# Kernel optimization log

Measured on AMD Instinct MI355X. Metric: run time of the kernel, lower is better.

Reference implementation:

```python
import jax, jax.numpy as jnp
import numpy as np
import math

N_QUBITS = 8
N_LAYERS = 2
EMBED = 512
HEADS = 64
B, T = 2, 1024


def _ry(state, theta, wire, off):
    # state: (batch?, 2, 2, ..., 2); theta: scalar or (N,)
    ax = off + wire
    st = jnp.moveaxis(state, ax, -1)
    s0, s1 = st[..., 0], st[..., 1]
    half = jnp.asarray(theta) * 0.5
    c, s = jnp.cos(half), jnp.sin(half)
    if c.ndim:  # batched angles -> broadcast over remaining qubit axes
        c = c.reshape((-1,) + (1,) * (s0.ndim - 1))
        s = s.reshape((-1,) + (1,) * (s0.ndim - 1))
    new = jnp.stack([c * s0 - s * s1, s * s0 + c * s1], axis=-1)
    return jnp.moveaxis(new, -1, ax)


def _cnot(state, cw, tw, off):
    st = jnp.moveaxis(state, (off + cw, off + tw), (-2, -1))
    new = jnp.stack([st[..., 0, :], st[..., 1, ::-1]], axis=-2)
    return jnp.moveaxis(new, (-2, -1), (off + cw, off + tw))


def _entangling_state(params):
    # Fixed-parameter block applied to |0...0>: single shared statevector.
    n = N_QUBITS
    psi = jnp.zeros((2,) * n, dtype=params.dtype).at[(0,) * n].set(1.0)
    for l in range(N_LAYERS):
        for q in range(n):
            psi = _ry(psi, params[l, q], q, 0)
        for q in range(n - 1):
            psi = _cnot(psi, q, q + 1, 0)
        psi = _cnot(psi, n - 1, 0, 0)
    return psi


def _quantum_heads(angles, params):
    # angles: (N, n_qubits) data-encoding RY angles; returns (N, n_qubits) <Z_q>.
    n = N_QUBITS
    psi0 = _entangling_state(params)
    state = jnp.broadcast_to(psi0, (angles.shape[0],) + (2,) * n)
    for q in range(n):
        state = _ry(state, angles[:, q], q, 1)
    probs = state * state  # real statevector -> probabilities
    zs = []
    for q in range(n):
        axes = tuple(a for a in range(1, n + 1) if a != q + 1)
        m = probs.sum(axes)  # (N, 2)
        zs.append(m[:, 0] - m[:, 1])
    return jnp.stack(zs, axis=-1)


def setup_inputs() -> dict:
    key = jax.random.key(0)
    kx, kq, kk, kv, kp = jax.random.split(key, 5)
    scale = 1.0 / math.sqrt(EMBED)
    return {
        "x": jax.random.normal(kx, (B, T, EMBED), dtype=jnp.float32),
        "Wq": jax.random.normal(kq, (EMBED, EMBED), dtype=jnp.float32) * scale,
        "Wk": jax.random.normal(kk, (EMBED, EMBED), dtype=jnp.float32) * scale,
        "Wv": jax.random.normal(kv, (EMBED, EMBED), dtype=jnp.float32) * scale,
        "params": jax.random.normal(kp, (N_LAYERS, N_QUBITS), dtype=jnp.float32),
    }


def reference(x, Wq, Wk, Wv, params):
    Bx, Tx, E = x.shape
    head_dim = E // HEADS
    q = x @ Wq.T
    k = x @ Wk.T
    v = x @ Wv.T
    # NOTE: attention on the full embed dim (no head split), scaled by sqrt(E).
    scores = jnp.einsum("bte,bse->bts", q, k) / jnp.sqrt(jnp.asarray(E, x.dtype))
    weights = jax.nn.softmax(scores, axis=-1)
    out = jnp.einsum("bts,bse->bte", weights, v)
    heads = out.reshape(Bx, Tx, HEADS, head_dim)[..., :N_QUBITS]
    angles = heads.reshape(-1, N_QUBITS)  # (B*T*HEADS, n_qubits)
    z = _quantum_heads(angles, params)
    return z.reshape(Bx, Tx, HEADS * N_QUBITS)
```

## Files before the change

### kernel.cpp

```cpp
#include <hip/hip_runtime.h>
#include <math.h>

typedef __attribute__((ext_vector_type(8))) short bf16x8;
typedef __attribute__((ext_vector_type(4))) float f32x4;

__device__ __forceinline__ ushort f2b(float f) {
    unsigned u = __float_as_uint(f);
    return (ushort)((u + 0x7FFFu + ((u >> 16) & 1u)) >> 16);
}

__device__ __forceinline__ void gl16(const ushort* g, ushort* l) {
    __builtin_amdgcn_global_load_lds((const __attribute__((address_space(1))) void*)g,
                                     (__attribute__((address_space(3))) void*)l, 16, 0, 0);
}

__device__ __forceinline__ void wait_pipe() { asm volatile("s_waitcnt vmcnt(4) lgkmcnt(0)" ::: "memory"); }
__device__ __forceinline__ void wait_all()  { asm volatile("s_waitcnt vmcnt(0) lgkmcnt(0)" ::: "memory"); }

__device__ __forceinline__ void stage64(const ushort* g, int ld, ushort* lds,
                                        int w, int lane) {
    const int rsub = lane >> 3;
    const size_t coff = (size_t)(((lane & 7) ^ (rsub & 7)) * 8);
#pragma unroll
    for (int ii = 0; ii < 2; ++ii) {
        const int i = w * 2 + ii;
        gl16(g + (size_t)(i * 8 + rsub) * ld + coff, lds + i * 512);
    }
}

__device__ __forceinline__ bf16x8 frag(const ushort* lds, int row0, int c, int lane) {
    const int r = row0 + (lane & 15);
    const int slot = (c * 4 + (lane >> 4)) ^ (r & 7);
    return *(const bf16x8*)(lds + (size_t)r * 64 + slot * 8);
}

__device__ __forceinline__ void compute64(const ushort* As, const ushort* Bs,
                                          f32x4 acc[2][2], int lane, int wr, int wc) {
#pragma unroll
    for (int c = 0; c < 2; ++c) {
        bf16x8 a[2], b[2];
#pragma unroll
        for (int f = 0; f < 2; ++f) {
            a[f] = frag(As, wr * 32 + f * 16, c, lane);
            b[f] = frag(Bs, wc * 32 + f * 16, c, lane);
        }
#pragma unroll
        for (int i = 0; i < 2; ++i)
#pragma unroll
            for (int j = 0; j < 2; ++j)
                acc[i][j] = __builtin_amdgcn_mfma_f32_16x16x32_bf16(a[i], b[j], acc[i][j], 0, 0, 0);
    }
}

__global__ __launch_bounds__(256) void cvtq_kernel(const float* __restrict__ x,
                                                   const float* __restrict__ wq,
                                                   const float* __restrict__ wk,
                                                   const float* __restrict__ wv,
                                                   const float* __restrict__ params,
                                                   ushort* __restrict__ xb,
                                                   ushort* __restrict__ wqb,
                                                   ushort* __restrict__ wkb,
                                                   ushort* __restrict__ wvb,
                                                   float* __restrict__ ab) {
    const int tid = threadIdx.x;
    if (blockIdx.y < 4) {
        const int z = blockIdx.y;
        const float* src = (z == 0) ? x : (z == 1) ? wq : (z == 2) ? wk : wv;
        ushort* dst = (z == 0) ? xb : (z == 1) ? wqb : (z == 2) ? wkb : wvb;
        const int n = (z == 0) ? (2048 * 512) : (512 * 512);
        const int i = (blockIdx.x * 256 + tid) * 8;
        if (i >= n) return;
        float4 v0 = *(const float4*)(src + i);
        float4 v1 = *(const float4*)(src + i + 4);
        ushort t[8] = {f2b(v0.x), f2b(v0.y), f2b(v0.z), f2b(v0.w),
                       f2b(v1.x), f2b(v1.y), f2b(v1.z), f2b(v1.w)};
        *(uint4*)(dst + i) = *(uint4*)t;
        return;
    }
    if (blockIdx.x != 0) return;
    __shared__ float st[256];
    __shared__ float red[64];
    st[tid] = (tid == 0) ? 1.0f : 0.0f;
    __syncthreads();
    for (int l = 0; l < 2; ++l) {
        for (int q = 0; q < 8; ++q) {
            float h = 0.5f * params[l * 8 + q];
            float c = cosf(h), s = sinf(h);
            int str = 1 << (7 - q);
            if ((tid & str) == 0) {
                float s0 = st[tid], s1 = st[tid + str];
                st[tid]       = c * s0 - s * s1;
                st[tid + str] = s * s0 + c * s1;
            }
            __syncthreads();
        }
        for (int q = 0; q < 8; ++q) {
            int cw = q, tw = (q + 1) & 7;
            int cs = 1 << (7 - cw), ts = 1 << (7 - tw);
            if ((tid & cs) && !(tid & ts)) {
                float a = st[tid], b = st[tid ^ ts];
                st[tid] = b;
                st[tid ^ ts] = a;
            }
            __syncthreads();
        }
    }
    const float amp = st[tid];
    float v[16];
#pragma unroll
    for (int q = 0; q < 8; ++q) {
        int str = 1 << (7 - q);
        v[q]     = amp * amp * ((tid & str) ? -1.0f : 1.0f);
        v[8 + q] = ((tid & str) == 0) ? 2.0f * amp * st[tid ^ str] : 0.0f;
    }
#pragma unroll
    for (int off = 32; off; off >>= 1)
#pragma unroll
        for (int q = 0; q < 16; ++q) v[q] += __shfl_xor(v[q], off);
    const int lane = tid & 63, wid = tid >> 6;
    if (lane == 0)
#pragma unroll
        for (int q = 0; q < 16; ++q) red[wid * 16 + q] = v[q];
    __syncthreads();
    if (tid < 16) ab[tid] = red[tid] + red[16 + tid] + red[32 + tid] + red[48 + tid];
}

__global__ __launch_bounds__(256) void qkv_mfma(const ushort* __restrict__ xb,
                                                const ushort* __restrict__ wqb,
                                                const ushort* __restrict__ wkb,
                                                const ushort* __restrict__ wvb,
                                                ushort* __restrict__ qb,
                                                ushort* __restrict__ kb,
                                                ushort* __restrict__ vT) {
    __shared__ ushort lds[3][2 * 64 * 64];
    const int tid = threadIdx.x, lane = tid & 63, w = tid >> 6;
    const int wr = w >> 1, wc = w & 1;
    const int z = blockIdx.z;
    int m0, n0, ldc;
    const ushort *A, *B;
    ushort* C;
    if (z < 2) {
        m0 = blockIdx.x << 6;  n0 = blockIdx.y << 6;
        A = xb;  B = (z == 0) ? wqb : wkb;  C = (z == 0) ? qb : kb;  ldc = 512;
    } else {
        m0 = blockIdx.y << 6;  n0 = blockIdx.x << 6;
        A = wvb;  B = xb;  C = vT;  ldc = 2048;
    }
    const ushort* Ap = A + (size_t)m0 * 512;
    const ushort* Bp = B + (size_t)n0 * 512;
    stage64(Ap, 512, lds[0], w, lane);
    stage64(Bp, 512, lds[0] + 4096, w, lane);
    stage64(Ap + 64, 512, lds[1], w, lane);
    stage64(Bp + 64, 512, lds[1] + 4096, w, lane);
    f32x4 acc[2][2] = {};
    const int NT = 8;
    for (int t = 0; t < NT; ++t) {
        if (t < NT - 1) wait_pipe(); else wait_all();
        __builtin_amdgcn_s_barrier();
        __builtin_amdgcn_sched_barrier(0);
        if (t + 2 < NT) {
            ushort* nb = lds[(t + 2) % 3];
            stage64(Ap + (t + 2) * 64, 512, nb, w, lane);
            stage64(Bp + (t + 2) * 64, 512, nb + 4096, w, lane);
        }
        const ushort* cb = lds[t % 3];
        compute64(cb, cb + 4096, acc, lane, wr, wc);
    }
    const int rb2 = (lane >> 4) << 2, cc = lane & 15;
#pragma unroll
    for (int fr = 0; fr < 2; ++fr)
#pragma unroll
        for (int fc = 0; fc < 2; ++fc) {
            int row = m0 + wr * 32 + fr * 16 + rb2;
            int col = n0 + wc * 32 + fc * 16 + cc;
#pragma unroll
            for (int r = 0; r < 4; ++r)
                C[(size_t)(row + r) * ldc + col] = f2b(acc[fr][fc][r]);
        }
}

__global__ __launch_bounds__(256) void scores_mfma(const ushort* __restrict__ qb,
                                                   const ushort* __restrict__ kb,
                                                   float* __restrict__ sb) {
    __shared__ ushort lds[3][2 * 64 * 64];
    const int tid = threadIdx.x, lane = tid & 63, w = tid >> 6;
    const int wr = w >> 1, wc = w & 1;
    const int m0 = blockIdx.x << 6, n0 = blockIdx.y << 6, z = blockIdx.z;
    const ushort* Ap = qb + (size_t)z * 1024 * 512 + (size_t)m0 * 512;
    const ushort* Bp = kb + (size_t)z * 1024 * 512 + (size_t)n0 * 512;
    float* C = sb + (size_t)z * 1024 * 1024;
    stage64(Ap, 512, lds[0], w, lane);
    stage64(Bp, 512, lds[0] + 4096, w, lane);
    stage64(Ap + 64, 512, lds[1], w, lane);
    stage64(Bp + 64, 512, lds[1] + 4096, w, lane);
    f32x4 acc[2][2] = {};
    const int NT = 8;
    for (int t = 0; t < NT; ++t) {
        if (t < NT - 1) wait_pipe(); else wait_all();
        __builtin_amdgcn_s_barrier();
        __builtin_amdgcn_sched_barrier(0);
        if (t + 2 < NT) {
            ushort* nb = lds[(t + 2) % 3];
            stage64(Ap + (t + 2) * 64, 512, nb, w, lane);
            stage64(Bp + (t + 2) * 64, 512, nb + 4096, w, lane);
        }
        const ushort* cb = lds[t % 3];
        compute64(cb, cb + 4096, acc, lane, wr, wc);
    }
    const float scale = 0.044194173824159216f;
    const int rb2 = (lane >> 4) << 2, cc = lane & 15;
#pragma unroll
    for (int fr = 0; fr < 2; ++fr)
#pragma unroll
        for (int fc = 0; fc < 2; ++fc) {
            int row = m0 + wr * 32 + fr * 16 + rb2;
            int col = n0 + wc * 32 + fc * 16 + cc;
#pragma unroll
            for (int r = 0; r < 4; ++r)
                C[(size_t)(row + r) * 1024 + col] = acc[fr][fc][r] * scale;
        }
}

__global__ __launch_bounds__(256) void softmax_kernel(const float* __restrict__ S,
                                                      ushort* __restrict__ W) {
    const int row = blockIdx.x, tid = threadIdx.x;
    const float* p = S + (size_t)row * 1024;
    float4 v = ((const float4*)p)[tid];
    float m = fmaxf(fmaxf(v.x, v.y), fmaxf(v.z, v.w));
#pragma unroll
    for (int off = 32; off; off >>= 1) m = fmaxf(m, __shfl_xor(m, off));
    __shared__ float sm[4];
    __shared__ float ss[4];
    const int wid = tid >> 6, lane = tid & 63;
    if (lane == 0) sm[wid] = m;
    __syncthreads();
    m = fmaxf(fmaxf(sm[0], sm[1]), fmaxf(sm[2], sm[3]));
    float e0 = expf(v.x - m), e1 = expf(v.y - m), e2 = expf(v.z - m), e3 = expf(v.w - m);
    float s = e0 + e1 + e2 + e3;
#pragma unroll
    for (int off = 32; off; off >>= 1) s += __shfl_xor(s, off);
    if (lane == 0) ss[wid] = s;
    __syncthreads();
    s = ss[0] + ss[1] + ss[2] + ss[3];
    float r = 1.0f / s;
    ushort4 o = {f2b(e0 * r), f2b(e1 * r), f2b(e2 * r), f2b(e3 * r)};
    ((ushort4*)(W + (size_t)row * 1024))[tid] = o;
}

__global__ __launch_bounds__(256) void pv_mfma(const ushort* __restrict__ wb,
                                               const ushort* __restrict__ vT,
                                               float* __restrict__ out,
                                               const float* __restrict__ ab) {
    __shared__ ushort lds[3][2 * 64 * 64];
    const int tid = threadIdx.x, lane = tid & 63, w = tid >> 6;
    const int wr = w >> 1, wc = w & 1;
    const int m0 = blockIdx.x << 6, n0 = blockIdx.y << 6, z = blockIdx.z;
    const ushort* Ap = wb + (size_t)z * 1024 * 1024 + (size_t)m0 * 1024;
    const ushort* Bp = vT + (size_t)n0 * 2048 + z * 1024;
    float* C = out + (size_t)z * 1024 * 512;
    stage64(Ap, 1024, lds[0], w, lane);
    stage64(Bp, 2048, lds[0] + 4096, w, lane);
    stage64(Ap + 64, 1024, lds[1], w, lane);
    stage64(Bp + 64, 2048, lds[1] + 4096, w, lane);
    f32x4 acc[2][2] = {};
    const int NT = 16;
    for (int t = 0; t < NT; ++t) {
        if (t < NT - 1) wait_pipe(); else wait_all();
        __builtin_amdgcn_s_barrier();
        __builtin_amdgcn_sched_barrier(0);
        if (t + 2 < NT) {
            ushort* nb = lds[(t + 2) % 3];
            stage64(Ap + (t + 2) * 64, 1024, nb, w, lane);
            stage64(Bp + (t + 2) * 64, 2048, nb + 4096, w, lane);
        }
        const ushort* cb = lds[t % 3];
        compute64(cb, cb + 4096, acc, lane, wr, wc);
    }
    const float Aq = ab[lane & 7], Bq = ab[8 + (lane & 7)];
    const int rb2 = (lane >> 4) << 2, cc = lane & 15;
#pragma unroll
    for (int fr = 0; fr < 2; ++fr)
#pragma unroll
        for (int fc = 0; fc < 2; ++fc) {
            int row = m0 + wr * 32 + fr * 16 + rb2;
            int col = n0 + wc * 32 + fc * 16 + cc;
#pragma unroll
            for (int r = 0; r < 4; ++r) {
                float sn, cs;
                sincosf(acc[fr][fc][r], &sn, &cs);
                C[(size_t)(row + r) * 512 + col] = cs * Aq - sn * Bq;
            }
        }
}

extern "C" void kernel_launch(void* const* d_in, const int* in_sizes, int n_in,
                              void* d_out, int out_size, void* d_ws, size_t ws_size,
                              hipStream_t stream) {
    const float* x      = (const float*)d_in[0];
    const float* Wq     = (const float*)d_in[1];
    const float* Wk     = (const float*)d_in[2];
    const float* Wv     = (const float*)d_in[3];
    const float* params = (const float*)d_in[4];
    float* out = (float*)d_out;

    char* base = (char*)d_ws;
    float*  ab  = (float*)base;
    ushort* xb  = (ushort*)(base + 256);
    ushort* wqb = xb + 2048 * 512;
    ushort* wkb = wqb + 512 * 512;
    ushort* wvb = wkb + 512 * 512;
    ushort* qb  = wvb + 512 * 512;
    ushort* kb  = qb + 2048 * 512;
    ushort* vT  = kb + 2048 * 512;
    float*  sb  = (float*)(vT + 2048 * 512);
    ushort* wb  = (ushort*)(sb + 2 * 1024 * 1024);

    hipLaunchKernelGGL(cvtq_kernel, dim3(512, 5), dim3(256), 0, stream,
                       x, Wq, Wk, Wv, params, xb, wqb, wkb, wvb, ab);
    hipLaunchKernelGGL(qkv_mfma, dim3(32, 8, 3), dim3(256), 0, stream,
                       xb, wqb, wkb, wvb, qb, kb, vT);
    hipLaunchKernelGGL(scores_mfma, dim3(16, 16, 2), dim3(256), 0, stream, qb, kb, sb);
    hipLaunchKernelGGL(softmax_kernel, dim3(2048), dim3(256), 0, stream, sb, wb);
    hipLaunchKernelGGL(pv_mfma, dim3(16, 8, 2), dim3(256), 0, stream, wb, vT, out, ab);
}
```

Baseline: 97.74 us.

## Fuse all stages into one cooperative persistent kernel with grid syncs

```diff
diff --git a/kernel.cpp b/kernel.cpp
--- a/kernel.cpp
+++ b/kernel.cpp
@@ -1,8 +1,13 @@
 #include <hip/hip_runtime.h>
+#include <hip/hip_cooperative_groups.h>
 #include <math.h>
+
+namespace cg = cooperative_groups;
 
 typedef __attribute__((ext_vector_type(8))) short bf16x8;
 typedef __attribute__((ext_vector_type(4))) float f32x4;
+
+#define GRID 512
 
 __device__ __forceinline__ ushort f2b(float f) {
     unsigned u = __float_as_uint(f);
@@ -52,35 +57,43 @@
     }
 }
 
-__global__ __launch_bounds__(256) void cvtq_kernel(const float* __restrict__ x,
-                                                   const float* __restrict__ wq,
-                                                   const float* __restrict__ wk,
-                                                   const float* __restrict__ wv,
-                                                   const float* __restrict__ params,
-                                                   ushort* __restrict__ xb,
-                                                   ushort* __restrict__ wqb,
-                                                   ushort* __restrict__ wkb,
-                                                   ushort* __restrict__ wvb,
-                                                   float* __restrict__ ab) {
-    const int tid = threadIdx.x;
-    if (blockIdx.y < 4) {
-        const int z = blockIdx.y;
-        const float* src = (z == 0) ? x : (z == 1) ? wq : (z == 2) ? wk : wv;
-        ushort* dst = (z == 0) ? xb : (z == 1) ? wqb : (z == 2) ? wkb : wvb;
-        const int n = (z == 0) ? (2048 * 512) : (512 * 512);
-        const int i = (blockIdx.x * 256 + tid) * 8;
-        if (i >= n) return;
-        float4 v0 = *(const float4*)(src + i);
-        float4 v1 = *(const float4*)(src + i + 4);
-        ushort t[8] = {f2b(v0.x), f2b(v0.y), f2b(v0.z), f2b(v0.w),
-                       f2b(v1.x), f2b(v1.y), f2b(v1.z), f2b(v1.w)};
-        *(uint4*)(dst + i) = *(uint4*)t;
-        return;
-    }
-    if (blockIdx.x != 0) return;
-    __shared__ float st[256];
-    __shared__ float red[64];
-    st[tid] = (tid == 0) ? 1.0f : 0.0f;
+__device__ __forceinline__ void gemm_tile(const ushort* Ap, const ushort* Bp,
+                                          int lda, int ldb, int NT, ushort* smem,
+                                          f32x4 acc[2][2], int tid) {
+    const int lane = tid & 63, w = tid >> 6, wr = w >> 1, wc = w & 1;
+    stage64(Ap, lda, smem, w, lane);
+    stage64(Bp, ldb, smem + 4096, w, lane);
+    stage64(Ap + 64, lda, smem + 8192, w, lane);
+    stage64(Bp + 64, ldb, smem + 8192 + 4096, w, lane);
+    for (int t = 0; t < NT; ++t) {
+        if (t < NT - 1) wait_pipe(); else wait_all();
+        __builtin_amdgcn_s_barrier();
+        __builtin_amdgcn_sched_barrier(0);
+        if (t + 2 < NT) {
+            ushort* nb = smem + ((t + 2) % 3) * 8192;
+            stage64(Ap + (t + 2) * 64, lda, nb, w, lane);
+            stage64(Bp + (t + 2) * 64, ldb, nb + 4096, w, lane);
+        }
+        const ushort* cb = smem + (t % 3) * 8192;
+        compute64(cb, cb + 4096, acc, lane, wr, wc);
+    }
+}
+
+__global__ __launch_bounds__(256, 2) void fused_all(
+        const float* __restrict__ x, const float* __restrict__ wq,
+        const float* __restrict__ wk, const float* __restrict__ wv,
+        const float* __restrict__ params, float* __restrict__ out,
+        ushort* xb, ushort* wqb, ushort* wkb, ushort* wvb,
+        ushort* qb, ushort* kb, ushort* vT, float* sb, ushort* wb) {
+    __shared__ ushort smem[3 * 8192];
+    const int tid = threadIdx.x, bid = blockIdx.x;
+    const int lane = tid & 63, wid = tid >> 6;
+    cg::grid_group grid = cg::this_grid();
+
+    float* stf  = (float*)smem;
+    float* redf = stf + 256;
+    float* abl  = redf + 64;
+    stf[tid] = (tid == 0) ? 1.0f : 0.0f;
     __syncthreads();
     for (int l = 0; l < 2; ++l) {
         for (int q = 0; q < 8; ++q) {
@@ -88,223 +101,185 @@
             float c = cosf(h), s = sinf(h);
             int str = 1 << (7 - q);
             if ((tid & str) == 0) {
-                float s0 = st[tid], s1 = st[tid + str];
-                st[tid]       = c * s0 - s * s1;
-                st[tid + str] = s * s0 + c * s1;
+                float s0 = stf[tid], s1 = stf[tid + str];
+                stf[tid]       = c * s0 - s * s1;
+                stf[tid + str] = s * s0 + c * s1;
             }
             __syncthreads();
         }
         for (int q = 0; q < 8; ++q) {
-            int cw = q, tw = (q + 1) & 7;
-            int cs = 1 << (7 - cw), ts = 1 << (7 - tw);
+            int tw = (q + 1) & 7;
+            int cs = 1 << (7 - q), ts = 1 << (7 - tw);
             if ((tid & cs) && !(tid & ts)) {
-                float a = st[tid], b = st[tid ^ ts];
-                st[tid] = b;
-                st[tid ^ ts] = a;
-            }
-            __syncthreads();
-        }
-    }
-    const float amp = st[tid];
-    float v[16];
+                float a = stf[tid], b = stf[tid ^ ts];
+                stf[tid] = b;
+                stf[tid ^ ts] = a;
+            }
+            __syncthreads();
+        }
+    }
+    const float amp = stf[tid];
+    float qv[16];
 #pragma unroll
     for (int q = 0; q < 8; ++q) {
         int str = 1 << (7 - q);
-        v[q]     = amp * amp * ((tid & str) ? -1.0f : 1.0f);
-        v[8 + q] = ((tid & str) == 0) ? 2.0f * amp * st[tid ^ str] : 0.0f;
+        qv[q]     = amp * amp * ((tid & str) ? -1.0f : 1.0f);
+        qv[8 + q] = ((tid & str) == 0) ? 2.0f * amp * stf[tid ^ str] : 0.0f;
     }
 #pragma unroll
     for (int off = 32; off; off >>= 1)
 #pragma unroll
-        for (int q = 0; q < 16; ++q) v[q] += __shfl_xor(v[q], off);
-    const int lane = tid & 63, wid = tid >> 6;
+        for (int q = 0; q < 16; ++q) qv[q] += __shfl_xor(qv[q], off);
     if (lane == 0)
 #pragma unroll
-        for (int q = 0; q < 16; ++q) red[wid * 16 + q] = v[q];
+        for (int q = 0; q < 16; ++q) redf[wid * 16 + q] = qv[q];
     __syncthreads();
-    if (tid < 16) ab[tid] = red[tid] + red[16 + tid] + red[32 + tid] + red[48 + tid];
-}
-
-__global__ __launch_bounds__(256) void qkv_mfma(const ushort* __restrict__ xb,
-                                                const ushort* __restrict__ wqb,
-                                                const ushort* __restrict__ wkb,
-                                                const ushort* __restrict__ wvb,
-                                                ushort* __restrict__ qb,
-                                                ushort* __restrict__ kb,
-                                                ushort* __restrict__ vT) {
-    __shared__ ushort lds[3][2 * 64 * 64];
-    const int tid = threadIdx.x, lane = tid & 63, w = tid >> 6;
-    const int wr = w >> 1, wc = w & 1;
-    const int z = blockIdx.z;
-    int m0, n0, ldc;
-    const ushort *A, *B;
-    ushort* C;
-    if (z < 2) {
-        m0 = blockIdx.x << 6;  n0 = blockIdx.y << 6;
-        A = xb;  B = (z == 0) ? wqb : wkb;  C = (z == 0) ? qb : kb;  ldc = 512;
-    } else {
-        m0 = blockIdx.y << 6;  n0 = blockIdx.x << 6;
-        A = wvb;  B = xb;  C = vT;  ldc = 2048;
-    }
-    const ushort* Ap = A + (size_t)m0 * 512;
-    const ushort* Bp = B + (size_t)n0 * 512;
-    stage64(Ap, 512, lds[0], w, lane);
-    stage64(Bp, 512, lds[0] + 4096, w, lane);
-    stage64(Ap + 64, 512, lds[1], w, lane);
-    stage64(Bp + 64, 512, lds[1] + 4096, w, lane);
-    f32x4 acc[2][2] = {};
-    const int NT = 8;
-    for (int t = 0; t < NT; ++t) {
-        if (t < NT - 1) wait_pipe(); else wait_all();
-        __builtin_amdgcn_s_barrier();
-        __builtin_amdgcn_sched_barrier(0);
-        if (t + 2 < NT) {
-            ushort* nb = lds[(t + 2) % 3];
-            stage64(Ap + (t + 2) * 64, 512, nb, w, lane);
-            stage64(Bp + (t + 2) * 64, 512, nb + 4096, w, lane);
-        }
-        const ushort* cb = lds[t % 3];
-        compute64(cb, cb + 4096, acc, lane, wr, wc);
-    }
-    const int rb2 = (lane >> 4) << 2, cc = lane & 15;
-#pragma unroll
-    for (int fr = 0; fr < 2; ++fr)
-#pragma unroll
-        for (int fc = 0; fc < 2; ++fc) {
-            int row = m0 + wr * 32 + fr * 16 + rb2;
-            int col = n0 + wc * 32 + fc * 16 + cc;
-#pragma unroll
-            for (int r = 0; r < 4; ++r)
-                C[(size_t)(row + r) * ldc + col] = f2b(acc[fr][fc][r]);
-        }
-}
-
-__global__ __launch_bounds__(256) void scores_mfma(const ushort* __restrict__ qb,
-                                                   const ushort* __restrict__ kb,
-                                                   float* __restrict__ sb) {
-    __shared__ ushort lds[3][2 * 64 * 64];
-    const int tid = threadIdx.x, lane = tid & 63, w = tid >> 6;
-    const int wr = w >> 1, wc = w & 1;
-    const int m0 = blockIdx.x << 6, n0 = blockIdx.y << 6, z = blockIdx.z;
-    const ushort* Ap = qb + (size_t)z * 1024 * 512 + (size_t)m0 * 512;
-    const ushort* Bp = kb + (size_t)z * 1024 * 512 + (size_t)n0 * 512;
-    float* C = sb + (size_t)z * 1024 * 1024;
-    stage64(Ap, 512, lds[0], w, lane);
-    stage64(Bp, 512, lds[0] + 4096, w, lane);
-    stage64(Ap + 64, 512, lds[1], w, lane);
-    stage64(Bp + 64, 512, lds[1] + 4096, w, lane);
-    f32x4 acc[2][2] = {};
-    const int NT = 8;
-    for (int t = 0; t < NT; ++t) {
-        if (t < NT - 1) wait_pipe(); else wait_all();
-        __builtin_amdgcn_s_barrier();
-        __builtin_amdgcn_sched_barrier(0);
-        if (t + 2 < NT) {
-            ushort* nb = lds[(t + 2) % 3];
-            stage64(Ap + (t + 2) * 64, 512, nb, w, lane);
-            stage64(Bp + (t + 2) * 64, 512, nb + 4096, w, lane);
-        }
-        const ushort* cb = lds[t % 3];
-        compute64(cb, cb + 4096, acc, lane, wr, wc);
-    }
-    const float scale = 0.044194173824159216f;
-    const int rb2 = (lane >> 4) << 2, cc = lane & 15;
-#pragma unroll
-    for (int fr = 0; fr < 2; ++fr)
-#pragma unroll
-        for (int fc = 0; fc < 2; ++fc) {
-            int row = m0 + wr * 32 + fr * 16 + rb2;
-            int col = n0 + wc * 32 + fc * 16 + cc;
-#pragma unroll
-            for (int r = 0; r < 4; ++r)
-                C[(size_t)(row + r) * 1024 + col] = acc[fr][fc][r] * scale;
-        }
-}
-
-__global__ __launch_bounds__(256) void softmax_kernel(const float* __restrict__ S,
-                                                      ushort* __restrict__ W) {
-    const int row = blockIdx.x, tid = threadIdx.x;
-    const float* p = S + (size_t)row * 1024;
-    float4 v = ((const float4*)p)[tid];
-    float m = fmaxf(fmaxf(v.x, v.y), fmaxf(v.z, v.w));
-#pragma unroll
-    for (int off = 32; off; off >>= 1) m = fmaxf(m, __shfl_xor(m, off));
-    __shared__ float sm[4];
-    __shared__ float ss[4];
-    const int wid = tid >> 6, lane = tid & 63;
-    if (lane == 0) sm[wid] = m;
+    if (tid < 16) abl[tid] = redf[tid] + redf[16 + tid] + redf[32 + tid] + redf[48 + tid];
     __syncthreads();
-    m = fmaxf(fmaxf(sm[0], sm[1]), fmaxf(sm[2], sm[3]));
-    float e0 = expf(v.x - m), e1 = expf(v.y - m), e2 = expf(v.z - m), e3 = expf(v.w - m);
-    float s = e0 + e1 + e2 + e3;
-#pragma unroll
-    for (int off = 32; off; off >>= 1) s += __shfl_xor(s, off);
-    if (lane == 0) ss[wid] = s;
-    __syncthreads();
-    s = ss[0] + ss[1] + ss[2] + ss[3];
-    float r = 1.0f / s;
-    ushort4 o = {f2b(e0 * r), f2b(e1 * r), f2b(e2 * r), f2b(e3 * r)};
-    ((ushort4*)(W + (size_t)row * 1024))[tid] = o;
-}
-
-__global__ __launch_bounds__(256) void pv_mfma(const ushort* __restrict__ wb,
-                                               const ushort* __restrict__ vT,
-                                               float* __restrict__ out,
-                                               const float* __restrict__ ab) {
-    __shared__ ushort lds[3][2 * 64 * 64];
-    const int tid = threadIdx.x, lane = tid & 63, w = tid >> 6;
-    const int wr = w >> 1, wc = w & 1;
-    const int m0 = blockIdx.x << 6, n0 = blockIdx.y << 6, z = blockIdx.z;
-    const ushort* Ap = wb + (size_t)z * 1024 * 1024 + (size_t)m0 * 1024;
-    const ushort* Bp = vT + (size_t)n0 * 2048 + z * 1024;
-    float* C = out + (size_t)z * 1024 * 512;
-    stage64(Ap, 1024, lds[0], w, lane);
-    stage64(Bp, 2048, lds[0] + 4096, w, lane);
-    stage64(Ap + 64, 1024, lds[1], w, lane);
-    stage64(Bp + 64, 2048, lds[1] + 4096, w, lane);
-    f32x4 acc[2][2] = {};
-    const int NT = 16;
-    for (int t = 0; t < NT; ++t) {
-        if (t < NT - 1) wait_pipe(); else wait_all();
-        __builtin_amdgcn_s_barrier();
-        __builtin_amdgcn_sched_barrier(0);
-        if (t + 2 < NT) {
-            ushort* nb = lds[(t + 2) % 3];
-            stage64(Ap + (t + 2) * 64, 1024, nb, w, lane);
-            stage64(Bp + (t + 2) * 64, 2048, nb + 4096, w, lane);
-        }
-        const ushort* cb = lds[t % 3];
-        compute64(cb, cb + 4096, acc, lane, wr, wc);
-    }
-    const float Aq = ab[lane & 7], Bq = ab[8 + (lane & 7)];
-    const int rb2 = (lane >> 4) << 2, cc = lane & 15;
-#pragma unroll
-    for (int fr = 0; fr < 2; ++fr)
-#pragma unroll
-        for (int fc = 0; fc < 2; ++fc) {
-            int row = m0 + wr * 32 + fr * 16 + rb2;
-            int col = n0 + wc * 32 + fc * 16 + cc;
-#pragma unroll
-            for (int r = 0; r < 4; ++r) {
-                float sn, cs;
-                sincosf(acc[fr][fc][r], &sn, &cs);
-                C[(size_t)(row + r) * 512 + col] = cs * Aq - sn * Bq;
-            }
-        }
+    const float Aq = abl[lane & 7], Bq = abl[8 + (lane & 7)];
+
+    const int CH = 131072 + 3 * 32768;
+    for (int c = bid * 256 + tid; c < CH; c += GRID * 256) {
+        const float* src; ushort* dst; int off;
+        if (c < 131072) { src = x; dst = xb; off = c * 8; }
+        else {
+            int c2 = c - 131072;
+            int wsel = c2 >> 15;
+            off = (c2 & 32767) * 8;
+            src = (wsel == 0) ? wq : (wsel == 1) ? wk : wv;
+            dst = (wsel == 0) ? wqb : (wsel == 1) ? wkb : wvb;
+        }
+        float4 v0 = *(const float4*)(src + off);
+        float4 v1 = *(const float4*)(src + off + 4);
+        ushort t8[8] = {f2b(v0.x), f2b(v0.y), f2b(v0.z), f2b(v0.w),
+                        f2b(v1.x), f2b(v1.y), f2b(v1.z), f2b(v1.w)};
+        *(uint4*)(dst + off) = *(uint4*)t8;
+    }
+    grid.sync();
+
+    for (int tt = bid; tt < 768; tt += GRID) {
+        const int z = tt >> 8, r = tt & 255;
+        int m0, n0, ldc;
+        const ushort *Ap, *Bp;
+        ushort* C;
+        if (z < 2) {
+            m0 = (r & 31) << 6;  n0 = (r >> 5) << 6;
+            Ap = xb + (size_t)m0 * 512;
+            Bp = (z ? wkb : wqb) + (size_t)n0 * 512;
+            C = z ? kb : qb;  ldc = 512;
+        } else {
+            m0 = (r >> 5) << 6;  n0 = (r & 31) << 6;
+            Ap = wvb + (size_t)m0 * 512;
+            Bp = xb + (size_t)n0 * 512;
+            C = vT;  ldc = 2048;
+        }
+        f32x4 acc[2][2] = {};
+        gemm_tile(Ap, Bp, 512, 512, 8, smem, acc, tid);
+        const int w = tid >> 6, wr = w >> 1, wc = w & 1;
+        const int rb2 = (lane >> 4) << 2, cc = lane & 15;
+#pragma unroll
+        for (int fr = 0; fr < 2; ++fr)
+#pragma unroll
+            for (int fc = 0; fc < 2; ++fc) {
+                int row = m0 + wr * 32 + fr * 16 + rb2;
+                int col = n0 + wc * 32 + fc * 16 + cc;
+#pragma unroll
+                for (int rr = 0; rr < 4; ++rr)
+                    C[(size_t)(row + rr) * ldc + col] = f2b(acc[fr][fc][rr]);
+            }
+        __syncthreads();
+    }
+    grid.sync();
+
+    {
+        const int z = bid >> 8, r = bid & 255;
+        const int m0 = (r & 15) << 6, n0 = (r >> 4) << 6;
+        const ushort* Ap = qb + (size_t)z * 524288 + (size_t)m0 * 512;
+        const ushort* Bp = kb + (size_t)z * 524288 + (size_t)n0 * 512;
+        float* C = sb + (size_t)z * 1048576;
+        f32x4 acc[2][2] = {};
+        gemm_tile(Ap, Bp, 512, 512, 8, smem, acc, tid);
+        const float scale = 0.044194173824159216f;
+        const int w = tid >> 6, wr = w >> 1, wc = w & 1;
+        const int rb2 = (lane >> 4) << 2, cc = lane & 15;
+#pragma unroll
+        for (int fr = 0; fr < 2; ++fr)
+#pragma unroll
+            for (int fc = 0; fc < 2; ++fc) {
+                int row = m0 + wr * 32 + fr * 16 + rb2;
+                int col = n0 + wc * 32 + fc * 16 + cc;
+#pragma unroll
+                for (int rr = 0; rr < 4; ++rr)
+                    C[(size_t)(row + rr) * 1024 + col] = acc[fr][fc][rr] * scale;
+            }
+    }
+    grid.sync();
+
+    {
+        float* sm = (float*)smem;
+        float* ss = sm + 4;
+        for (int row = bid; row < 2048; row += GRID) {
+            const float* p = sb + (size_t)row * 1024;
+            float4 v = ((const float4*)p)[tid];
+            float m = fmaxf(fmaxf(v.x, v.y), fmaxf(v.z, v.w));
+#pragma unroll
+            for (int off = 32; off; off >>= 1) m = fmaxf(m, __shfl_xor(m, off));
+            if (lane == 0) sm[wid] = m;
+            __syncthreads();
+            m = fmaxf(fmaxf(sm[0], sm[1]), fmaxf(sm[2], sm[3]));
+            float e0 = expf(v.x - m), e1 = expf(v.y - m);
+            float e2 = expf(v.z - m), e3 = expf(v.w - m);
+            float s = e0 + e1 + e2 + e3;
+#pragma unroll
+            for (int off = 32; off; off >>= 1) s += __shfl_xor(s, off);
+            if (lane == 0) ss[wid] = s;
+            __syncthreads();
+            s = ss[0] + ss[1] + ss[2] + ss[3];
+            float rr = 1.0f / s;
+            ushort4 o = {f2b(e0 * rr), f2b(e1 * rr), f2b(e2 * rr), f2b(e3 * rr)};
+            ((ushort4*)(wb + (size_t)row * 1024))[tid] = o;
+            __syncthreads();
+        }
+    }
+    grid.sync();
+
+    if (bid < 256) {
+        const int z = bid >> 7, r = bid & 127;
+        const int m0 = (r & 15) << 6, n0 = (r >> 4) << 6;
+        const ushort* Ap = wb + (size_t)z * 1048576 + (size_t)m0 * 1024;
+        const ushort* Bp = vT + (size_t)n0 * 2048 + z * 1024;
+        float* C = out + (size_t)z * 524288;
+        f32x4 acc[2][2] = {};
+        gemm_tile(Ap, Bp, 1024, 2048, 16, smem, acc, tid);
+        const int w = tid >> 6, wr = w >> 1, wc = w & 1;
+        const int rb2 = (lane >> 4) << 2, cc = lane & 15;
+#pragma unroll
+        for (int fr = 0; fr < 2; ++fr)
+#pragma unroll
+            for (int fc = 0; fc < 2; ++fc) {
+                int row = m0 + wr * 32 + fr * 16 + rb2;
+                int col = n0 + wc * 32 + fc * 16 + cc;
+#pragma unroll
+                for (int rr = 0; rr < 4; ++rr) {
+                    float sn, cs;
+                    sincosf(acc[fr][fc][rr], &sn, &cs);
+                    C[(size_t)(row + rr) * 512 + col] = cs * Aq - sn * Bq;
+                }
+            }
+    }
 }
 
 extern "C" void kernel_launch(void* const* d_in, const int* in_sizes, int n_in,
                               void* d_out, int out_size, void* d_ws, size_t ws_size,
                               hipStream_t stream) {
     const float* x      = (const float*)d_in[0];
-    const float* Wq     = (const float*)d_in[1];
-    const float* Wk     = (const float*)d_in[2];
-    const float* Wv     = (const float*)d_in[3];
+    const float* wq     = (const float*)d_in[1];
+    const float* wk     = (const float*)d_in[2];
+    const float* wv     = (const float*)d_in[3];
     const float* params = (const float*)d_in[4];
     float* out = (float*)d_out;
 
     char* base = (char*)d_ws;
-    float*  ab  = (float*)base;
     ushort* xb  = (ushort*)(base + 256);
     ushort* wqb = xb + 2048 * 512;
     ushort* wkb = wqb + 512 * 512;
@@ -315,11 +290,11 @@
     float*  sb  = (float*)(vT + 2048 * 512);
     ushort* wb  = (ushort*)(sb + 2 * 1024 * 1024);
 
-    hipLaunchKernelGGL(cvtq_kernel, dim3(512, 5), dim3(256), 0, stream,
-                       x, Wq, Wk, Wv, params, xb, wqb, wkb, wvb, ab);
-    hipLaunchKernelGGL(qkv_mfma, dim3(32, 8, 3), dim3(256), 0, stream,
-                       xb, wqb, wkb, wvb, qb, kb, vT);
-    hipLaunchKernelGGL(scores_mfma, dim3(16, 16, 2), dim3(256), 0, stream, qb, kb, sb);
-    hipLaunchKernelGGL(softmax_kernel, dim3(2048), dim3(256), 0, stream, sb, wb);
-    hipLaunchKernelGGL(pv_mfma, dim3(16, 8, 2), dim3(256), 0, stream, wb, vT, out, ab);
-}
+    void* args[15] = {
+        (void*)&x, (void*)&wq, (void*)&wk, (void*)&wv, (void*)&params,
+        (void*)&out, (void*)&xb, (void*)&wqb, (void*)&wkb, (void*)&wvb,
+        (void*)&qb, (void*)&kb, (void*)&vT, (void*)&sb, (void*)&wb
+    };
+    hipLaunchCooperativeKernel((const void*)fused_all, dim3(GRID), dim3(256),
+                               args, 0, stream);
+}
```

Measured after the change: 365.4 us. 3.74x slower.
